# Kernel tuning notes

Measured on AMD Instinct MI355X. Metric: run time of the kernel, lower is better.

## Reference

```python
import jax, jax.numpy as jnp
import numpy as np

N_EXPERTS = 8
Z_DIM = 128
HID = 1024
OUT = 3072  # e.g. 3x32x32 flattened generator output
BATCH = 2048


def hash_vectors(z, n):
    """Deterministic per-sample hash -> expert index in [0, n).

    Proxy for the repo's hash_vectors (which hashes the latent vector):
    quantize |z|, sum over feature dim, mod n. Non-differentiable by design.
    """
    return jnp.mod(jnp.floor(jnp.abs(z) * 1000.0).sum(axis=1).astype(jnp.int32), n)


def setup_inputs() -> dict:
    key = jax.random.key(0)
    kz, k1, kb1, k2, kb2 = jax.random.split(key, 5)
    z = jax.random.normal(kz, (BATCH, Z_DIM), dtype=jnp.float32)
    s1 = 1.0 / np.sqrt(Z_DIM)
    s2 = 1.0 / np.sqrt(HID)
    # Stacked per-expert MLP params (each expert independently initialized,
    # mirroring reset_parameters on each deepcopy).
    W1 = jax.random.uniform(k1, (N_EXPERTS, Z_DIM, HID), jnp.float32, -s1, s1)
    b1 = jax.random.uniform(kb1, (N_EXPERTS, HID), jnp.float32, -s1, s1)
    W2 = jax.random.uniform(k2, (N_EXPERTS, HID, OUT), jnp.float32, -s2, s2)
    b2 = jax.random.uniform(kb2, (N_EXPERTS, OUT), jnp.float32, -s2, s2)
    return {"z": z, "W1": W1, "b1": b1, "W2": W2, "b2": b2}


def reference(z, W1, b1, W2, b2):
    # Hard routing: each sample i goes to expert idx[i].
    idx = hash_vectors(z, N_EXPERTS)  # [B]
    # Dense compute-all-experts then select (vectorized replacement for the
    # per-sample Python loop in the original forward).
    h = jax.nn.relu(jnp.einsum('bi,eih->beh', z, W1) + b1[None, :, :])  # [B,E,H]
    y = jnp.einsum('beh,eho->beo', h, W2) + b2[None, :, :]              # [B,E,O]
    out = jnp.take_along_axis(y, idx[:, None, None], axis=1)[:, 0, :]   # [B,O]
    return out
```

## Files before the change

kernel.cpp:

```cpp
#include <hip/hip_runtime.h>
#include <hip/hip_bf16.h>
#include <hip/hip_cooperative_groups.h>

namespace cg = cooperative_groups;


#define BATCH 2048
#define ZD 128
#define HID 1024
#define OUTD 3072
#define NEXP 8
#define MAXTF 24
#define NRB (BATCH / 32)

typedef short bf16x8 __attribute__((ext_vector_type(8)));
typedef float f32x4 __attribute__((ext_vector_type(4)));

#define BAR_NODRAIN()                                             \
    do {                                                          \
        asm volatile("s_waitcnt lgkmcnt(0)" ::: "memory");        \
        __builtin_amdgcn_s_barrier();                             \
        asm volatile("" ::: "memory");                            \
    } while (0)


__global__ __launch_bounds__(256) void routescan_kernel(
    const float* __restrict__ z, __hip_bfloat16* __restrict__ zb,
    int* __restrict__ pcnt, int* __restrict__ ntl,
    int* __restrict__ texp, int* __restrict__ perm) {
    __shared__ int lcnt[NEXP];
    __shared__ int se[32], sp[32];
    __shared__ int base_s[NEXP];
    __shared__ int soff_s[NEXP + 1];

    int t = threadIdx.x, bid = blockIdx.x;
    if (t < NEXP) lcnt[t] = 0;
    __syncthreads();

    int s = bid * 32 + (t >> 3);
    int li = t & 7;
    const float* zp = z + (size_t)s * ZD + li * 16;
    float sum = 0.f;
    union { bf16x8 v8; __hip_bfloat16 h[8]; } u0, u1;
#pragma unroll
    for (int i = 0; i < 4; i++) {
        float4 v = ((const float4*)zp)[i];
        sum += floorf(fabsf(v.x) * 1000.0f) + floorf(fabsf(v.y) * 1000.0f) +
               floorf(fabsf(v.z) * 1000.0f) + floorf(fabsf(v.w) * 1000.0f);
        __hip_bfloat16* dst = (i < 2) ? &u0.h[i * 4] : &u1.h[(i - 2) * 4];
        dst[0] = __float2bfloat16(v.x);
        dst[1] = __float2bfloat16(v.y);
        dst[2] = __float2bfloat16(v.z);
        dst[3] = __float2bfloat16(v.w);
    }
    bf16x8* zo = (bf16x8*)(zb + (size_t)s * ZD + li * 16);
    zo[0] = u0.v8;
    zo[1] = u1.v8;

    sum += __shfl_down(sum, 4);
    sum += __shfl_down(sum, 2);
    sum += __shfl_down(sum, 1);
    if (li == 0) {
        int e = ((int)sum) & 7;
        int lpos = atomicAdd(&lcnt[e], 1);
        se[t >> 3] = e;
        sp[t >> 3] = lpos;
    }
    __syncthreads();
    if (t < NEXP) pcnt[bid * NEXP + t] = lcnt[t];

    cg::this_grid().sync();

    if (t < NEXP) {
        int tot = 0, pre = 0;
#pragma unroll 1
        for (int b = 0; b < NRB; ++b) {
            int c = pcnt[b * NEXP + t];
            if (b < bid) pre += c;
            tot += c;
        }
        lcnt[t] = tot;
        base_s[t] = pre;
    }
    __syncthreads();
    if (t == 0) {
        int o = 0;
        for (int e = 0; e < NEXP; e++) {
            soff_s[e] = o;
            o += (lcnt[e] + 127) & ~127;
        }
        soff_s[NEXP] = o;
    }
    __syncthreads();

    if (t < 32) {
        int e = se[t];
        perm[soff_s[e] + base_s[e] + sp[t]] = bid * 32 + t;
    }

    if (bid == 0) {
        int total = soff_s[NEXP];
        if (t == 0) *ntl = total / 128;
        for (int tt = t; tt < total / 128; tt += 256) {
            int r = tt * 128, e = 0;
            while (r >= soff_s[e + 1]) e++;
            texp[tt] = e;
        }
        for (int r = t; r < total; r += 256) {
            int e = 0;
            while (r >= soff_s[e + 1]) e++;
            if (r - soff_s[e] >= lcnt[e]) perm[r] = -1;
        }
    }
}

__global__ __launch_bounds__(256, 4) void gemm1_fast(
    const __hip_bfloat16* __restrict__ zb, const float* __restrict__ W1,
    const float* __restrict__ b1, const int* __restrict__ ntl,
    const int* __restrict__ texp, const int* __restrict__ perm,
    __hip_bfloat16* __restrict__ H) {
    int mt = blockIdx.y;
    if (mt >= 2 * (*ntl)) return;
    int e = texp[mt >> 1];
    int n0 = blockIdx.x * 64;

    __shared__ __align__(16) __hip_bfloat16 As[2][64 * 64];
    __shared__ __align__(16) __hip_bfloat16 Bs[2][64 * 64];

    int tid = threadIdx.x;
    int lane = tid & 63, wave = tid >> 6;
    int cc = lane & 15, q = lane >> 4;
    int mw = (wave >> 1) * 32, nw = (wave & 1) * 32;

    int sc = tid & 7, rg = tid >> 3;
    int r0 = perm[mt * 64 + rg];      if (r0 < 0) r0 = 0;
    int r1 = perm[mt * 64 + rg + 32]; if (r1 < 0) r1 = 0;
    const __hip_bfloat16* Ap0 = zb + (size_t)r0 * ZD + sc * 8;
    const __hip_bfloat16* Ap1 = zb + (size_t)r1 * ZD + sc * 8;
    int awb = rg * 64 + (sc ^ (rg & 7)) * 8;

    int bkc = tid & 7, bn2 = (tid >> 3) * 2;
    const float* Bgf = W1 + (size_t)e * ZD * HID + (size_t)(bkc * 8) * HID + n0 + bn2;
    int bwb[2];
#pragma unroll
    for (int j = 0; j < 2; j++)
        bwb[j] = ((bn2 + j) * 8 + (bkc ^ ((bn2 + j) & 7))) * 8;

    int A0 = (mw + cc) * 64, B0 = (nw + cc) * 64;
    int X0 = (q ^ (cc & 7)) * 8, X1 = ((4 + q) ^ (cc & 7)) * 8;

    float bias[2];
#pragma unroll
    for (int j = 0; j < 2; j++) bias[j] = b1[(size_t)e * HID + n0 + nw + j * 16 + cc];

    f32x4 zero4 = {0.f, 0.f, 0.f, 0.f};
    f32x4 acc[2][2];
#pragma unroll
    for (int i = 0; i < 2; i++)
#pragma unroll
        for (int j = 0; j < 2; j++) acc[i][j] = zero4;

    bf16x8 ga0 = *(const bf16x8*)Ap0;
    bf16x8 ga1 = *(const bf16x8*)Ap1;
    float2 braw[8];
#pragma unroll
    for (int i = 0; i < 8; i++) braw[i] = *(const float2*)(Bgf + (size_t)i * HID);

#pragma unroll
    for (int it = 0; it < 2; ++it) {
        __hip_bfloat16* Ac = As[it];
        __hip_bfloat16* Bc = Bs[it];
        union { bf16x8 v8; __hip_bfloat16 h[8]; } gbv[2];
#pragma unroll
        for (int i = 0; i < 8; i++) {
            gbv[0].h[i] = __float2bfloat16(braw[i].x);
            gbv[1].h[i] = __float2bfloat16(braw[i].y);
        }
        *(bf16x8*)(Ac + awb) = ga0;
        *(bf16x8*)(Ac + awb + 2048) = ga1;
#pragma unroll
        for (int j = 0; j < 2; j++) *(bf16x8*)(Bc + bwb[j]) = gbv[j].v8;
        if (it == 0) {
            ga0 = *(const bf16x8*)(Ap0 + 64);
            ga1 = *(const bf16x8*)(Ap1 + 64);
#pragma unroll
            for (int i = 0; i < 8; i++)
                braw[i] = *(const float2*)(Bgf + (size_t)(64 + i) * HID);
        }
        BAR_NODRAIN();
#pragma unroll
        for (int kh = 0; kh < 2; ++kh) {
            int X = kh ? X1 : X0;
            bf16x8 af[2], bfr[2];
#pragma unroll
            for (int i = 0; i < 2; i++) af[i] = *(const bf16x8*)(Ac + A0 + i * 1024 + X);
#pragma unroll
            for (int j = 0; j < 2; j++) bfr[j] = *(const bf16x8*)(Bc + B0 + j * 1024 + X);
#pragma unroll
            for (int i = 0; i < 2; i++)
#pragma unroll
                for (int j = 0; j < 2; j++)
                    acc[i][j] = __builtin_amdgcn_mfma_f32_16x16x32_bf16(af[i], bfr[j],
                                                                        acc[i][j], 0, 0, 0);
        }
    }
#pragma unroll
    for (int i = 0; i < 2; i++)
#pragma unroll
        for (int r = 0; r < 4; r++) {
            int m = mw + i * 16 + q * 4 + r;
            __hip_bfloat16* hp = H + (size_t)(mt * 64 + m) * HID + n0 + nw + cc;
#pragma unroll
            for (int j = 0; j < 2; j++)
                hp[j * 16] = __float2bfloat16(fmaxf(acc[i][j][r] + bias[j], 0.f));
        }
}

__global__ __launch_bounds__(256, 2) void gemm2_fast(
    const __hip_bfloat16* __restrict__ H, const float* __restrict__ W2,
    const float* __restrict__ b2, const int* __restrict__ ntl,
    const int* __restrict__ texp, const int* __restrict__ perm,
    float* __restrict__ out) {
    int mt = blockIdx.y;
    if (mt >= *ntl) return;
    int e = texp[mt];
    int n0 = blockIdx.x * 128;

    __shared__ __align__(16) __hip_bfloat16 As[2][128 * 64];
    __shared__ __align__(16) __hip_bfloat16 Bs[2][128 * 64];
    __shared__ int rows_s[128];

    int tid = threadIdx.x;
    if (tid < 128) rows_s[tid] = perm[mt * 128 + tid];

    int lane = tid & 63, wave = tid >> 6;
    int cc = lane & 15, q = lane >> 4;
    int mw = (wave >> 1) * 64, nw = (wave & 1) * 64;

    int sr = tid >> 3, sc = tid & 7;
    int awbase = sr * 64 + (sc ^ (sr & 7)) * 8;
    const __hip_bfloat16* Ag = H + ((size_t)mt * 128 + sr) * HID + sc * 8;

    int bkc = tid & 7, bn = (tid >> 3) * 4;
    const float* Bgf = W2 + (size_t)e * HID * OUTD + (size_t)(bkc * 8) * OUTD + n0 + bn;
    int bwb[4];
#pragma unroll
    for (int j = 0; j < 4; j++)
        bwb[j] = (bn + j) * 64 + ((bkc ^ ((bn + j) & 7))) * 8;

    int A0 = (mw + cc) * 64, B0 = (nw + cc) * 64;
    int X0 = (q ^ (cc & 7)) * 8, X1 = ((4 + q) ^ (cc & 7)) * 8;

    float bias[4];
#pragma unroll
    for (int j = 0; j < 4; j++) bias[j] = b2[(size_t)e * OUTD + n0 + nw + j * 16 + cc];

    f32x4 zero4 = {0.f, 0.f, 0.f, 0.f};
    f32x4 acc[4][4];
#pragma unroll
    for (int i = 0; i < 4; i++)
#pragma unroll
        for (int j = 0; j < 4; j++) acc[i][j] = zero4;

    bf16x8 gaA[4], gaB[4];
    float4 brA[8], brB[8];
#pragma unroll
    for (int p = 0; p < 4; p++) gaA[p] = *(const bf16x8*)(Ag + (size_t)p * 32 * HID);
#pragma unroll
    for (int i = 0; i < 8; i++) brA[i] = *(const float4*)(Bgf + (size_t)i * OUTD);
#pragma unroll
    for (int p = 0; p < 4; p++) gaB[p] = *(const bf16x8*)(Ag + (size_t)p * 32 * HID + 64);
#pragma unroll
    for (int i = 0; i < 8; i++) brB[i] = *(const float4*)(Bgf + (size_t)(64 + i) * OUTD);

    const int NIT = HID / 64;
    for (int itp = 0; itp < NIT / 2; ++itp) {
        int kre = itp * 128;
        bool more = (itp < NIT / 2 - 1);

        {
            union { bf16x8 v8; __hip_bfloat16 h[8]; } gb[4];
#pragma unroll
            for (int i = 0; i < 8; i++) {
                gb[0].h[i] = __float2bfloat16(brA[i].x);
                gb[1].h[i] = __float2bfloat16(brA[i].y);
                gb[2].h[i] = __float2bfloat16(brA[i].z);
                gb[3].h[i] = __float2bfloat16(brA[i].w);
            }
#pragma unroll
            for (int p = 0; p < 4; p++) *(bf16x8*)(As[0] + awbase + p * 2048) = gaA[p];
#pragma unroll
            for (int j = 0; j < 4; j++) *(bf16x8*)(Bs[0] + bwb[j]) = gb[j].v8;
            if (more) {
#pragma unroll
                for (int p = 0; p < 4; p++)
                    gaA[p] = *(const bf16x8*)(Ag + (size_t)p * 32 * HID + kre + 128);
#pragma unroll
                for (int i = 0; i < 8; i++)
                    brA[i] = *(const float4*)(Bgf + (size_t)(kre + 128 + i) * OUTD);
            }
            BAR_NODRAIN();
#pragma unroll
            for (int kh = 0; kh < 2; ++kh) {
                int X = kh ? X1 : X0;
                bf16x8 af[4], bfr[4];
#pragma unroll
                for (int i = 0; i < 4; i++) af[i] = *(const bf16x8*)(As[0] + A0 + i * 1024 + X);
#pragma unroll
                for (int j = 0; j < 4; j++) bfr[j] = *(const bf16x8*)(Bs[0] + B0 + j * 1024 + X);
#pragma unroll
                for (int i = 0; i < 4; i++)
#pragma unroll
                    for (int j = 0; j < 4; j++)
                        acc[i][j] = __builtin_amdgcn_mfma_f32_16x16x32_bf16(af[i], bfr[j],
                                                                            acc[i][j], 0, 0, 0);
            }
        }

        {
            union { bf16x8 v8; __hip_bfloat16 h[8]; } gb[4];
#pragma unroll
            for (int i = 0; i < 8; i++) {
                gb[0].h[i] = __float2bfloat16(brB[i].x);
                gb[1].h[i] = __float2bfloat16(brB[i].y);
                gb[2].h[i] = __float2bfloat16(brB[i].z);
                gb[3].h[i] = __float2bfloat16(brB[i].w);
            }
#pragma unroll
            for (int p = 0; p < 4; p++) *(bf16x8*)(As[1] + awbase + p * 2048) = gaB[p];
#pragma unroll
            for (int j = 0; j < 4; j++) *(bf16x8*)(Bs[1] + bwb[j]) = gb[j].v8;
            if (more) {
#pragma unroll
                for (int p = 0; p < 4; p++)
                    gaB[p] = *(const bf16x8*)(Ag + (size_t)p * 32 * HID + kre + 192);
#pragma unroll
                for (int i = 0; i < 8; i++)
                    brB[i] = *(const float4*)(Bgf + (size_t)(kre + 192 + i) * OUTD);
            }
            BAR_NODRAIN();
#pragma unroll
            for (int kh = 0; kh < 2; ++kh) {
                int X = kh ? X1 : X0;
                bf16x8 af[4], bfr[4];
#pragma unroll
                for (int i = 0; i < 4; i++) af[i] = *(const bf16x8*)(As[1] + A0 + i * 1024 + X);
#pragma unroll
                for (int j = 0; j < 4; j++) bfr[j] = *(const bf16x8*)(Bs[1] + B0 + j * 1024 + X);
#pragma unroll
                for (int i = 0; i < 4; i++)
#pragma unroll
                    for (int j = 0; j < 4; j++)
                        acc[i][j] = __builtin_amdgcn_mfma_f32_16x16x32_bf16(af[i], bfr[j],
                                                                            acc[i][j], 0, 0, 0);
            }
        }
    }

#pragma unroll
    for (int i = 0; i < 4; i++)
#pragma unroll
        for (int r = 0; r < 4; r++) {
            int m = mw + i * 16 + q * 4 + r;
            int orow = rows_s[m];
            if (orow >= 0) {
                float* op = out + (size_t)orow * OUTD + n0 + nw + cc;
#pragma unroll
                for (int j = 0; j < 4; j++) op[j * 16] = acc[i][j][r] + bias[j];
            }
        }
}

extern "C" void kernel_launch(void* const* d_in, const int* in_sizes, int n_in,
                              void* d_out, int out_size, void* d_ws, size_t ws_size,
                              hipStream_t stream) {
    const float* z  = (const float*)d_in[0];
    const float* W1 = (const float*)d_in[1];
    const float* b1 = (const float*)d_in[2];
    const float* W2 = (const float*)d_in[3];
    const float* b2 = (const float*)d_in[4];
    float* out = (float*)d_out;

    char* ws = (char*)d_ws;
    int* ntl    = (int*)(ws + 64);
    int* texp   = (int*)(ws + 128);
    int* perm   = (int*)(ws + 256);
    int* pcnt   = (int*)(ws + 12544);
    __hip_bfloat16* zb  = (__hip_bfloat16*)(ws + 78080);
    __hip_bfloat16* Hb  = (__hip_bfloat16*)(ws + 602368);

    void* kargs[] = {(void*)&z, (void*)&zb, (void*)&pcnt,
                     (void*)&ntl, (void*)&texp, (void*)&perm};
    hipLaunchCooperativeKernel((const void*)routescan_kernel, dim3(NRB), dim3(256),
                               kargs, 0, stream);
    hipLaunchKernelGGL(gemm1_fast, dim3(HID / 64, 2 * MAXTF), dim3(256), 0, stream,
                       zb, W1, b1, ntl, texp, perm, Hb);
    hipLaunchKernelGGL(gemm2_fast, dim3(OUTD / 128, MAXTF), dim3(256), 0, stream,
                       Hb, W2, b2, ntl, texp, perm, out);
}
```

Baseline: 232.5 us.

## Replace cooperative grid sync with last-block-done atomic counter in routing scan

After: 202.1 us. 13.1% less time.

```diff
diff --git a/kernel.cpp b/kernel.cpp
--- a/kernel.cpp
+++ b/kernel.cpp
@@ -1,8 +1,5 @@
 #include <hip/hip_runtime.h>
 #include <hip/hip_bf16.h>
-#include <hip/hip_cooperative_groups.h>
-
-namespace cg = cooperative_groups;
 
 
 #define BATCH 2048
@@ -26,12 +23,12 @@
 
 __global__ __launch_bounds__(256) void routescan_kernel(
     const float* __restrict__ z, __hip_bfloat16* __restrict__ zb,
-    int* __restrict__ pcnt, int* __restrict__ ntl,
-    int* __restrict__ texp, int* __restrict__ perm) {
+    int* __restrict__ pcnt, int* __restrict__ eidx, int* __restrict__ done,
+    int* __restrict__ ntl, int* __restrict__ texp, int* __restrict__ perm) {
     __shared__ int lcnt[NEXP];
-    __shared__ int se[32], sp[32];
-    __shared__ int base_s[NEXP];
+    __shared__ int sp[NRB * NEXP];
     __shared__ int soff_s[NEXP + 1];
+    __shared__ int lastflag;
 
     int t = threadIdx.x, bid = blockIdx.x;
     if (t < NEXP) lcnt[t] = 0;
@@ -63,24 +60,30 @@
     if (li == 0) {
         int e = ((int)sum) & 7;
         int lpos = atomicAdd(&lcnt[e], 1);
-        se[t >> 3] = e;
-        sp[t >> 3] = lpos;
+        eidx[s] = e | (lpos << 3);
     }
     __syncthreads();
     if (t < NEXP) pcnt[bid * NEXP + t] = lcnt[t];
 
-    cg::this_grid().sync();
-
+    __threadfence();
+    if (t == 0) {
+        int old = atomicAdd(done, 1);
+        lastflag = (((old + 1) & (NRB - 1)) == 0) ? 1 : 0;
+    }
+    __syncthreads();
+    if (!lastflag) return;
+    __threadfence();
+
+    for (int i = t; i < NRB * NEXP; i += 256) sp[i] = pcnt[i];
+    __syncthreads();
     if (t < NEXP) {
-        int tot = 0, pre = 0;
-#pragma unroll 1
+        int run = 0;
         for (int b = 0; b < NRB; ++b) {
-            int c = pcnt[b * NEXP + t];
-            if (b < bid) pre += c;
-            tot += c;
-        }
-        lcnt[t] = tot;
-        base_s[t] = pre;
+            int c = sp[b * NEXP + t];
+            sp[b * NEXP + t] = run;
+            run += c;
+        }
+        lcnt[t] = run;
     }
     __syncthreads();
     if (t == 0) {
@@ -90,27 +93,21 @@
             o += (lcnt[e] + 127) & ~127;
         }
         soff_s[NEXP] = o;
-    }
-    __syncthreads();
-
-    if (t < 32) {
-        int e = se[t];
-        perm[soff_s[e] + base_s[e] + sp[t]] = bid * 32 + t;
-    }
-
-    if (bid == 0) {
-        int total = soff_s[NEXP];
-        if (t == 0) *ntl = total / 128;
-        for (int tt = t; tt < total / 128; tt += 256) {
-            int r = tt * 128, e = 0;
-            while (r >= soff_s[e + 1]) e++;
-            texp[tt] = e;
-        }
-        for (int r = t; r < total; r += 256) {
-            int e = 0;
-            while (r >= soff_s[e + 1]) e++;
-            if (r - soff_s[e] >= lcnt[e]) perm[r] = -1;
-        }
+        *ntl = o / 128;
+    }
+    __syncthreads();
+    int total = soff_s[NEXP];
+    for (int r = t; r < total; r += 256) perm[r] = -1;
+    for (int tt = t; tt < total / 128; tt += 256) {
+        int r = tt * 128, e = 0;
+        while (r >= soff_s[e + 1]) e++;
+        texp[tt] = e;
+    }
+    __syncthreads();
+    for (int ss = t; ss < BATCH; ss += 256) {
+        int pk = eidx[ss];
+        int e = pk & 7, lpos = pk >> 3, b = ss >> 5;
+        perm[soff_s[e] + sp[b * NEXP + e] + lpos] = ss;
     }
 }
 
@@ -382,17 +379,17 @@
     float* out = (float*)d_out;
 
     char* ws = (char*)d_ws;
+    int* done   = (int*)ws;
     int* ntl    = (int*)(ws + 64);
     int* texp   = (int*)(ws + 128);
     int* perm   = (int*)(ws + 256);
-    int* pcnt   = (int*)(ws + 12544);
+    int* eidx   = (int*)(ws + 12544);
+    int* pcnt   = (int*)(ws + 24576);
     __hip_bfloat16* zb  = (__hip_bfloat16*)(ws + 78080);
     __hip_bfloat16* Hb  = (__hip_bfloat16*)(ws + 602368);
 
-    void* kargs[] = {(void*)&z, (void*)&zb, (void*)&pcnt,
-                     (void*)&ntl, (void*)&texp, (void*)&perm};
-    hipLaunchCooperativeKernel((const void*)routescan_kernel, dim3(NRB), dim3(256),
-                               kargs, 0, stream);
+    hipLaunchKernelGGL(routescan_kernel, dim3(NRB), dim3(256), 0, stream,
+                       z, zb, pcnt, eidx, done, ntl, texp, perm);
     hipLaunchKernelGGL(gemm1_fast, dim3(HID / 64, 2 * MAXTF), dim3(256), 0, stream,
                        zb, W1, b1, ntl, texp, perm, Hb);
     hipLaunchKernelGGL(gemm2_fast, dim3(OUTD / 128, MAXTF), dim3(256), 0, stream,
```
